# Kernel tuning notes

Hardware: AMD Instinct MI355X
Metric: run time of the kernel (lower is better)

Reference implementation:

```python
import jax, jax.numpy as jnp
import numpy as np

B1, B2, R, L, D, H = 48, 48, 36, 30, 1024, 4
EPS = 1e-8


def _l2norm(x):
    return x / (jnp.sqrt(jnp.sum(x * x, axis=-1, keepdims=True)) + EPS)


def _summary_attn(x, w1, b1, w2, b2):
    # x: (B1,B2,N,D). MLP scores -> softmax over N -> weighted mean over H heads.
    h = jax.nn.relu(jnp.einsum('abnd,ed->abne', x, w1) + b1)
    s = jnp.einsum('abne,he->abnh', h, w2) + b2          # (B1,B2,N,H)
    p = jax.nn.softmax(jnp.swapaxes(s, -1, -2), axis=-1)  # (B1,B2,H,N)
    w = jnp.einsum('abhn,abnd->abhd', p, x)               # (B1,B2,H,D)
    return w.mean(axis=-2)                                # (B1,B2,D)


def setup_inputs() -> dict:
    key = jax.random.key(0)
    ks = jax.random.split(key, 12)
    r = np.sqrt(6.0) / np.sqrt(D + D)  # xavier uniform as in init_weights
    return {
        'v1': jax.random.normal(ks[0], (B1, R, D), dtype=jnp.float32),
        'v2': jax.random.normal(ks[1], (B2, L, D), dtype=jnp.float32),
        'w_img': jax.random.uniform(ks[2], (D, D), jnp.float32, -r, r),
        'w_txt': jax.random.uniform(ks[3], (D, D), jnp.float32, -r, r),
        'w1a': jax.random.normal(ks[4], (D, D), jnp.float32) * 0.02,
        'b1a': jnp.zeros((D,), jnp.float32),
        'w2a': jax.random.normal(ks[5], (H, D), jnp.float32) * 0.02,
        'b2a': jnp.zeros((H,), jnp.float32),
        'w1b': jax.random.normal(ks[6], (D, D), jnp.float32) * 0.02,
        'b1b': jnp.zeros((D,), jnp.float32),
        'w2b': jax.random.normal(ks[7], (H, D), jnp.float32) * 0.02,
        'b2b': jnp.zeros((H,), jnp.float32),
    }


def reference(v1, v2, w_img, w_txt, w1a, b1a, w2a, b2a, w1b, b1b, w2b, b2b):
    d = v1.shape[-1]
    inv_sqrt_d = np.float32(1.0 / np.sqrt(d))
    k1 = jnp.einsum('ard,ed->are', v1, w_img)  # (B1,R,D)
    k2 = jnp.einsum('bld,ed->ble', v2, w_txt)  # (B2,L,D)

    # qkv_attention(k2, k1, v1): queries=words, keys/values=regions
    s1 = jnp.einsum('bld,ard->ablr', k2, k1) * inv_sqrt_d   # (B1,B2,L,R)
    p1 = jax.nn.softmax(s1, axis=-1)
    fused_v2 = jnp.einsum('ablr,ard->abld', p1, v1)         # weighted_v1 -> fused_v2

    # qkv_attention(k1, k2, v2): queries=regions, keys/values=words
    s2 = jnp.einsum('ard,bld->abrl', k1, k2) * inv_sqrt_d   # (B1,B2,R,L)
    p2 = jax.nn.softmax(s2, axis=-1)
    fused_v1 = jnp.einsum('abrl,bld->abrd', p2, v2)         # weighted_v2 -> fused_v1

    co_v1 = _l2norm(_summary_attn(fused_v1, w1a, b1a, w2a, b2a))
    co_v2 = _l2norm(_summary_attn(fused_v2, w1b, b1b, w2b, b2b))
    return jnp.sum(co_v1 * co_v2, axis=-1)  # (B1,B2) score matrix
```

## Files before the change

kernel.cpp:

```cpp
#include <hip/hip_runtime.h>

#define D 1024
#define NB1 48
#define NB2 48
#define RR 36
#define LL 30
#define NH 4

typedef short bf16x8 __attribute__((ext_vector_type(8)));
typedef float f32x4 __attribute__((ext_vector_type(4)));
typedef unsigned short u16x8 __attribute__((ext_vector_type(8)));

#define MFMA16(a, b, c) __builtin_amdgcn_mfma_f32_16x16x32_bf16(a, b, c, 0, 0, 0)

__device__ __forceinline__ unsigned short f2bf(float x) {
  unsigned u = __float_as_uint(x);
  u += 0x7FFF + ((u >> 16) & 1);
  return (unsigned short)(u >> 16);
}
__device__ __forceinline__ float bf2f(unsigned short h) {
  return __uint_as_float(((unsigned)h) << 16);
}
__device__ __forceinline__ void split8(const float* v, bf16x8& h8, bf16x8& l8) {
  u16x8 hi, lo;
#pragma unroll
  for (int i = 0; i < 8; ++i) {
    unsigned short h = f2bf(v[i]);
    hi[i] = h;
    lo[i] = f2bf(v[i] - bf2f(h));
  }
  h8 = __builtin_bit_cast(bf16x8, hi);
  l8 = __builtin_bit_cast(bf16x8, lo);
}

__device__ __forceinline__ void conv_body(const float* __restrict__ X,
                                          unsigned short* __restrict__ out,
                                          int rows, int g) {
  const int lane = threadIdx.x & 63;
  const int tile = g >> 5, kc = g & 31;
  const int row = tile * 16 + (lane & 15);
  const int k = kc * 32 + (lane >> 4) * 8;
  float v[8];
  if (row < rows) {
    const float4* s = (const float4*)(X + (size_t)row * 1024 + k);
    float4 x0 = s[0], x1 = s[1];
    v[0] = x0.x; v[1] = x0.y; v[2] = x0.z; v[3] = x0.w;
    v[4] = x1.x; v[5] = x1.y; v[6] = x1.z; v[7] = x1.w;
  } else {
#pragma unroll
    for (int i = 0; i < 8; ++i) v[i] = 0.f;
  }
  bf16x8 hi, lo;
  split8(v, hi, lo);
  bf16x8* o = (bf16x8*)(out + (size_t)g * 1024 + lane * 8);
  o[0] = hi;
  o[64] = lo;
}

__global__ __launch_bounds__(256) void conv6(
    const float* __restrict__ v1, const float* __restrict__ v2,
    const float* __restrict__ wimg, const float* __restrict__ wtxt,
    const float* __restrict__ w1a, const float* __restrict__ w1b,
    unsigned short* v1f, unsigned short* v2f, unsigned short* wimgf,
    unsigned short* wtxtf, unsigned short* w1af, unsigned short* w1bf) {
  const float* X; unsigned short* O; int rows;
  switch (blockIdx.y) {
    case 0: X = v1; O = v1f; rows = 1728; break;
    case 1: X = v2; O = v2f; rows = 1440; break;
    case 2: X = wimg; O = wimgf; rows = 1024; break;
    case 3: X = wtxt; O = wtxtf; rows = 1024; break;
    case 4: X = w1a; O = w1af; rows = 1024; break;
    default: X = w1b; O = w1bf; rows = 1024; break;
  }
  const int tiles = (rows + 15) >> 4;
  const int g = blockIdx.x * 4 + (threadIdx.x >> 6);
  if (g >= tiles * 32) return;
  conv_body(X, O, rows, g);
}

__global__ __launch_bounds__(256) void conv_k(const float* __restrict__ k1,
                                              const float* __restrict__ k2,
                                              unsigned short* k1f, unsigned short* k2f) {
  const float* X = blockIdx.y ? k2 : k1;
  unsigned short* O = blockIdx.y ? k2f : k1f;
  const int rows = blockIdx.y ? 1440 : 1728;
  const int tiles = (rows + 15) >> 4;
  const int g = blockIdx.x * 4 + (threadIdx.x >> 6);
  if (g >= tiles * 32) return;
  conv_body(X, O, rows, g);
}

__global__ __launch_bounds__(256) void convG(const float* __restrict__ G2a,
                                             const float* __restrict__ G1b,
                                             unsigned short* G2aF, unsigned short* G1bF) {
  const int t = threadIdx.x, lane = t & 63;
  const int bb = blockIdx.x >> 4;
  const int nt = ((blockIdx.x & 15) << 2) + (t >> 6);
  const int c = lane & 15, q = lane >> 4;
  if (blockIdx.y == 0) {
    float v[8];
#pragma unroll
    for (int j = 0; j < 8; ++j) {
      int l = q * 8 + j;
      v[j] = (l < LL) ? G2a[(size_t)(bb * LL + l) * D + nt * 16 + c] : 0.f;
    }
    bf16x8 hi, lo;
    split8(v, hi, lo);
    bf16x8* o = (bf16x8*)(G2aF + ((size_t)(bb * 64 + nt) * 2) * 512 + lane * 8);
    o[0] = hi;
    o[64] = lo;
  } else {
#pragma unroll
    for (int kc = 0; kc < 2; ++kc) {
      float v[8];
#pragma unroll
      for (int j = 0; j < 8; ++j) {
        int r = kc * 32 + q * 8 + j;
        v[j] = (r < RR) ? G1b[(size_t)(bb * RR + r) * D + nt * 16 + c] : 0.f;
      }
      bf16x8 hi, lo;
      split8(v, hi, lo);
      bf16x8* o = (bf16x8*)(G1bF + (((size_t)(bb * 64 + nt) * 2 + kc) * 2) * 512 + lane * 8);
      o[0] = hi;
      o[64] = lo;
    }
  }
}

__device__ __forceinline__ void gemm4_body(const bf16x8* __restrict__ Af,
                                           const bf16x8* __restrict__ Bf,
                                           float* __restrict__ C,
                                           int M, int N, float scale,
                                           int Mtiles, int Ntiles) {
  const int lane = threadIdx.x & 63;
  const int w = threadIdx.x >> 6;
  const int mb = blockIdx.y * 8 + (w >> 1) * 4;
  const int nb = blockIdx.x * 8 + (w & 1) * 4;
  size_t ab[4], bb[4];
#pragma unroll
  for (int i = 0; i < 4; ++i) {
    int tm = mb + i; if (tm > Mtiles - 1) tm = Mtiles - 1;
    ab[i] = (size_t)tm * 4096 + lane;
    int tn = nb + i; if (tn > Ntiles - 1) tn = Ntiles - 1;
    bb[i] = (size_t)tn * 4096 + lane;
  }
  f32x4 acc[4][4];
#pragma unroll
  for (int i = 0; i < 4; ++i)
#pragma unroll
    for (int j = 0; j < 4; ++j) acc[i][j] = (f32x4){0.f, 0.f, 0.f, 0.f};
#pragma unroll 1
  for (int kc = 0; kc < 32; ++kc) {
    bf16x8 ah[4], al[4], bh[4], bl[4];
#pragma unroll
    for (int i = 0; i < 4; ++i) { ah[i] = Af[ab[i]]; al[i] = Af[ab[i] + 64]; ab[i] += 128; }
#pragma unroll
    for (int j = 0; j < 4; ++j) { bh[j] = Bf[bb[j]]; bl[j] = Bf[bb[j] + 64]; bb[j] += 128; }
#pragma unroll
    for (int i = 0; i < 4; ++i)
#pragma unroll
      for (int j = 0; j < 4; ++j) {
        acc[i][j] = MFMA16(ah[i], bh[j], acc[i][j]);
        acc[i][j] = MFMA16(al[i], bh[j], acc[i][j]);
        acc[i][j] = MFMA16(ah[i], bl[j], acc[i][j]);
      }
  }
  const int c16 = lane & 15, q = lane >> 4;
#pragma unroll
  for (int i = 0; i < 4; ++i) {
#pragma unroll
    for (int reg = 0; reg < 4; ++reg) {
      int r = (mb + i) * 16 + q * 4 + reg;
      if (r < M) {
#pragma unroll
        for (int j = 0; j < 4; ++j) {
          int col = (nb + j) * 16 + c16;
          if (col < N) C[(size_t)r * N + col] = acc[i][j][reg] * scale;
        }
      }
    }
  }
}

__global__ __launch_bounds__(256) void proj_fused(
    const bf16x8* __restrict__ v1f, const bf16x8* __restrict__ v2f,
    const bf16x8* __restrict__ wimgf, const bf16x8* __restrict__ wtxtf,
    const bf16x8* __restrict__ w1af, const bf16x8* __restrict__ w1bf,
    float* k1, float* k2, float* G2a, float* G1b) {
  const int z = blockIdx.z;
  const bf16x8* Af = (z == 0 || z == 3) ? v1f : v2f;
  const bf16x8* Bf = (z == 0) ? wimgf : (z == 1) ? wtxtf : (z == 2) ? w1af : w1bf;
  float* C = (z == 0) ? k1 : (z == 1) ? k2 : (z == 2) ? G2a : G1b;
  const int M = (z == 0 || z == 3) ? 1728 : 1440;
  const int Mt = (z == 0 || z == 3) ? 108 : 92;
  if ((int)blockIdx.y * 8 >= Mt) return;
  gemm4_body(Af, Bf, C, M, 1024, 1.f, Mt, 64);
}

__global__ __launch_bounds__(256) void cross_fused(
    const bf16x8* __restrict__ k2f, const bf16x8* __restrict__ k1f,
    const bf16x8* __restrict__ v2f, const bf16x8* __restrict__ v1f,
    float* Sbuf, float* Cbuf) {
  if (blockIdx.z == 0) gemm4_body(k2f, k1f, Sbuf, 1440, 1728, 0.03125f, 92, 108);
  else                 gemm4_body(v2f, v1f, Cbuf, 1440, 1728, 1.f, 92, 108);
}

__global__ __launch_bounds__(256) void gram_partial(const float* __restrict__ v1,
                                                    const float* __restrict__ v2,
                                                    float* __restrict__ pg) {
  const int y = blockIdx.y, cx = blockIdx.x;
  const int isV1 = y < 48;
  const int batch = isV1 ? y : y - 48;
  const int Nr = isV1 ? RR : LL;
  const float* base = isV1 ? v1 + (size_t)batch * RR * D : v2 + (size_t)batch * LL * D;
  __shared__ __align__(16) float vs[36][132];
  const int t = threadIdx.x;
  for (int idx = t; idx < Nr * 32; idx += 256) {
    int row = idx >> 5, c4 = idx & 31;
    *(float4*)&vs[row][c4 * 4] = *(const float4*)&base[(size_t)row * D + cx * 128 + c4 * 4];
  }
  __syncthreads();
  const int nt3 = Nr / 3;
  float acc[3][3] = {{0.f,0.f,0.f},{0.f,0.f,0.f},{0.f,0.f,0.f}};
  const int i0 = (t / nt3) * 3, j0 = (t - (t / nt3) * nt3) * 3;
  if (t < nt3 * nt3) {
    for (int k4 = 0; k4 < 32; ++k4) {
      float4 a[3], b[3];
#pragma unroll
      for (int ii = 0; ii < 3; ++ii) a[ii] = *(const float4*)&vs[i0 + ii][k4 * 4];
#pragma unroll
      for (int jj = 0; jj < 3; ++jj) b[jj] = *(const float4*)&vs[j0 + jj][k4 * 4];
#pragma unroll
      for (int ii = 0; ii < 3; ++ii)
#pragma unroll
        for (int jj = 0; jj < 3; ++jj) {
          acc[ii][jj] = fmaf(a[ii].x, b[jj].x, acc[ii][jj]);
          acc[ii][jj] = fmaf(a[ii].y, b[jj].y, acc[ii][jj]);
          acc[ii][jj] = fmaf(a[ii].z, b[jj].z, acc[ii][jj]);
          acc[ii][jj] = fmaf(a[ii].w, b[jj].w, acc[ii][jj]);
        }
    }
    float* o = pg + ((size_t)y * 8 + cx) * 1296;
#pragma unroll
    for (int ii = 0; ii < 3; ++ii)
#pragma unroll
      for (int jj = 0; jj < 3; ++jj) o[(i0 + ii) * Nr + (j0 + jj)] = acc[ii][jj];
  }
}

__global__ __launch_bounds__(256) void gram_reduce(const float* __restrict__ pg,
                                                   float* __restrict__ g11,
                                                   float* __restrict__ g22) {
  const int y = blockIdx.x;
  const int isV1 = y < 48;
  const int batch = isV1 ? y : y - 48;
  const int NN = isV1 ? RR * RR : LL * LL;
  const float* p = pg + (size_t)y * 8 * 1296;
  float* o = isV1 ? g11 + (size_t)batch * RR * RR : g22 + (size_t)batch * LL * LL;
  for (int i = threadIdx.x; i < NN; i += 256) {
    float s = 0.f;
#pragma unroll
    for (int c = 0; c < 8; ++c) s += p[c * 1296 + i];
    o[i] = s;
  }
}

__global__ __launch_bounds__(256) void pair_kernel(
    const float* __restrict__ Sb, const float* __restrict__ Cb,
    const bf16x8* __restrict__ G2aF, const bf16x8* __restrict__ G1bF,
    const float* __restrict__ g22, const float* __restrict__ g11,
    const float* __restrict__ b1a, const float* __restrict__ w2a, const float* __restrict__ b2a,
    const float* __restrict__ b1b, const float* __restrict__ w2b, const float* __restrict__ b2b,
    float* __restrict__ out) {
  const int pair = blockIdx.x;
  const int a = pair / NB2;
  const int b = pair - a * NB2;
  const int t = threadIdx.x, lane = t & 63, w = t >> 6;
  const int c16 = lane & 15, q = lane >> 4;

  __shared__ __align__(16) float sS[LL][RR];
  __shared__ __align__(16) float p2s[48][36];
  __shared__ __align__(16) float p1s[32][68];
  __shared__ float red[4][48][NH];
  __shared__ float sa[RR][NH];
  __shared__ float sbm[LL][NH];
  __shared__ float qa[RR], qb[LL], u1[RR], u2[LL];
  __shared__ float redbuf[3][4];

  for (int i = t; i < 48 * 36; i += 256) ((float*)p2s)[i] = 0.f;
  for (int i = t; i < 32 * 68; i += 256) ((float*)p1s)[i] = 0.f;
  for (int i = t; i < LL * RR; i += 256) {
    int l = i / RR, r = i - l * RR;
    sS[l][r] = Sb[(size_t)(b * LL + l) * 1728 + a * RR + r];
  }
  __syncthreads();

  if (t < LL) {
    float m = -1e30f;
    for (int r = 0; r < RR; ++r) m = fmaxf(m, sS[t][r]);
    float s = 0.f;
    for (int r = 0; r < RR; ++r) { float e = __expf(sS[t][r] - m); p1s[t][r] = e; s += e; }
    float inv = 1.f / s;
    for (int r = 0; r < RR; ++r) p1s[t][r] *= inv;
  } else if (t >= 64 && t < 64 + RR) {
    int r = t - 64;
    float m = -1e30f;
    for (int l = 0; l < LL; ++l) m = fmaxf(m, sS[l][r]);
    float s = 0.f;
    for (int l = 0; l < LL; ++l) { float e = __expf(sS[l][r] - m); p2s[r][l] = e; s += e; }
    float inv = 1.f / s;
    for (int l = 0; l < LL; ++l) p2s[r][l] *= inv;
  }
  __syncthreads();

  bf16x8 pAh[3], pAl[3];
#pragma unroll
  for (int mt = 0; mt < 3; ++mt) {
    float v[8];
    const float* rp = &p2s[mt * 16 + c16][q * 8];
    float4 x0 = *(const float4*)rp;
    float4 x1 = *(const float4*)(rp + 4);
    v[0] = x0.x; v[1] = x0.y; v[2] = x0.z; v[3] = x0.w;
    v[4] = x1.x; v[5] = x1.y; v[6] = x1.z; v[7] = x1.w;
    split8(v, pAh[mt], pAl[mt]);
  }
  float scA[3][4][NH];
#pragma unroll
  for (int mt = 0; mt < 3; ++mt)
#pragma unroll
    for (int reg = 0; reg < 4; ++reg)
#pragma unroll
      for (int h = 0; h < NH; ++h) scA[mt][reg][h] = 0.f;

  for (int nt = w; nt < 64; nt += 4) {
    const bf16x8* gp = G2aF + ((size_t)(b * 64 + nt) * 2) * 64 + lane;
    bf16x8 Bh = gp[0], Bl = gp[64];
    const int col = nt * 16 + c16;
    const float bias = b1a[col];
    const float w0 = w2a[col], w1 = w2a[D + col], w2v = w2a[2 * D + col], w3 = w2a[3 * D + col];
#pragma unroll
    for (int mt = 0; mt < 3; ++mt) {
      f32x4 acc = {bias, bias, bias, bias};
      acc = MFMA16(pAh[mt], Bh, acc);
      acc = MFMA16(pAl[mt], Bh, acc);
      acc = MFMA16(pAh[mt], Bl, acc);
#pragma unroll
      for (int reg = 0; reg < 4; ++reg) {
        float hv = fmaxf(acc[reg], 0.f);
        scA[mt][reg][0] = fmaf(hv, w0, scA[mt][reg][0]);
        scA[mt][reg][1] = fmaf(hv, w1, scA[mt][reg][1]);
        scA[mt][reg][2] = fmaf(hv, w2v, scA[mt][reg][2]);
        scA[mt][reg][3] = fmaf(hv, w3, scA[mt][reg][3]);
      }
    }
  }
#pragma unroll
  for (int mt = 0; mt < 3; ++mt)
#pragma unroll
    for (int reg = 0; reg < 4; ++reg)
#pragma unroll
      for (int h = 0; h < NH; ++h) {
        float v = scA[mt][reg][h];
        v += __shfl_xor(v, 1);
        v += __shfl_xor(v, 2);
        v += __shfl_xor(v, 4);
        v += __shfl_xor(v, 8);
        if (c16 == 0) red[w][mt * 16 + q * 4 + reg][h] = v;
      }
  __syncthreads();
  if (t < RR * NH) {
    int r = t >> 2, h = t & 3;
    sa[r][h] = red[0][r][h] + red[1][r][h] + red[2][r][h] + red[3][r][h] + b2a[h];
  }
  __syncthreads();

  bf16x8 pBh[2][2], pBl[2][2];
#pragma unroll
  for (int mt = 0; mt < 2; ++mt)
#pragma unroll
    for (int kc = 0; kc < 2; ++kc) {
      float v[8];
      const float* rp = &p1s[mt * 16 + c16][kc * 32 + q * 8];
      float4 x0 = *(const float4*)rp;
      float4 x1 = *(const float4*)(rp + 4);
      v[0] = x0.x; v[1] = x0.y; v[2] = x0.z; v[3] = x0.w;
      v[4] = x1.x; v[5] = x1.y; v[6] = x1.z; v[7] = x1.w;
      split8(v, pBh[mt][kc], pBl[mt][kc]);
    }
  float scB[2][4][NH];
#pragma unroll
  for (int mt = 0; mt < 2; ++mt)
#pragma unroll
    for (int reg = 0; reg < 4; ++reg)
#pragma unroll
      for (int h = 0; h < NH; ++h) scB[mt][reg][h] = 0.f;

  for (int nt = w; nt < 64; nt += 4) {
    const bf16x8* gp = G1bF + (((size_t)(a * 64 + nt) * 2) * 2) * 64 + lane;
    bf16x8 B0h = gp[0], B0l = gp[64], B1h = gp[128], B1l = gp[192];
    const int col = nt * 16 + c16;
    const float bias = b1b[col];
    const float w0 = w2b[col], w1 = w2b[D + col], w2v = w2b[2 * D + col], w3 = w2b[3 * D + col];
#pragma unroll
    for (int mt = 0; mt < 2; ++mt) {
      f32x4 acc = {bias, bias, bias, bias};
      acc = MFMA16(pBh[mt][0], B0h, acc);
      acc = MFMA16(pBl[mt][0], B0h, acc);
      acc = MFMA16(pBh[mt][0], B0l, acc);
      acc = MFMA16(pBh[mt][1], B1h, acc);
      acc = MFMA16(pBl[mt][1], B1h, acc);
      acc = MFMA16(pBh[mt][1], B1l, acc);
#pragma unroll
      for (int reg = 0; reg < 4; ++reg) {
        float hv = fmaxf(acc[reg], 0.f);
        scB[mt][reg][0] = fmaf(hv, w0, scB[mt][reg][0]);
        scB[mt][reg][1] = fmaf(hv, w1, scB[mt][reg][1]);
        scB[mt][reg][2] = fmaf(hv, w2v, scB[mt][reg][2]);
        scB[mt][reg][3] = fmaf(hv, w3, scB[mt][reg][3]);
      }
    }
  }
#pragma unroll
  for (int mt = 0; mt < 2; ++mt)
#pragma unroll
    for (int reg = 0; reg < 4; ++reg)
#pragma unroll
      for (int h = 0; h < NH; ++h) {
        float v = scB[mt][reg][h];
        v += __shfl_xor(v, 1);
        v += __shfl_xor(v, 2);
        v += __shfl_xor(v, 4);
        v += __shfl_xor(v, 8);
        if (c16 == 0) red[w][mt * 16 + q * 4 + reg][h] = v;
      }
  __syncthreads();
  if (t < LL * NH) {
    int l = t >> 2, h = t & 3;
    sbm[l][h] = red[0][l][h] + red[1][l][h] + red[2][l][h] + red[3][l][h] + b2b[h];
  }
  __syncthreads();

  if (t < NH) {
    const int h = t;
    float m = -1e30f;
    for (int r = 0; r < RR; ++r) m = fmaxf(m, sa[r][h]);
    float s = 0.f;
    for (int r = 0; r < RR; ++r) { float e = __expf(sa[r][h] - m); sa[r][h] = e; s += e; }
    float inv = 1.f / s;
    for (int r = 0; r < RR; ++r) sa[r][h] *= inv;
  } else if (t >= 64 && t < 64 + NH) {
    const int h = t - 64;
    float m = -1e30f;
    for (int l = 0; l < LL; ++l) m = fmaxf(m, sbm[l][h]);
    float s = 0.f;
    for (int l = 0; l < LL; ++l) { float e = __expf(sbm[l][h] - m); sbm[l][h] = e; s += e; }
    float inv = 1.f / s;
    for (int l = 0; l < LL; ++l) sbm[l][h] *= inv;
  }
  __syncthreads();
  if (t < RR) qa[t] = 0.25f * (sa[t][0] + sa[t][1] + sa[t][2] + sa[t][3]);
  else if (t >= 64 && t < 64 + LL) {
    int l = t - 64;
    qb[l] = 0.25f * (sbm[l][0] + sbm[l][1] + sbm[l][2] + sbm[l][3]);
  }
  __syncthreads();

  if (t < LL) {
    float x = 0.f;
    for (int r = 0; r < RR; ++r) x = fmaf(qa[r], p2s[r][t], x);
    u2[t] = x;
  } else if (t >= 64 && t < 64 + RR) {
    int r = t - 64;
    float x = 0.f;
    for (int l = 0; l < LL; ++l) x = fmaf(qb[l], p1s[l][r], x);
    u1[r] = x;
  }
  __syncthreads();

  float pnum = 0.f, pn1 = 0.f, pn2 = 0.f;
  {
    const float* Cab = Cb + (size_t)(b * LL) * 1728 + a * RR;
    for (int i = t; i < LL * RR; i += 256) {
      int l = i / RR, r = i - l * RR;
      pnum = fmaf(u2[l] * u1[r], Cab[(size_t)l * 1728 + r], pnum);
    }
    const float* G22 = g22 + (size_t)b * LL * LL;
    for (int i = t; i < LL * LL; i += 256) {
      int l = i / LL, l2 = i - l * LL;
      pn1 = fmaf(u2[l] * u2[l2], G22[i], pn1);
    }
    const float* G11 = g11 + (size_t)a * RR * RR;
    for (int i = t; i < RR * RR; i += 256) {
      int r = i / RR, r2 = i - r * RR;
      pn2 = fmaf(u1[r] * u1[r2], G11[i], pn2);
    }
  }
#pragma unroll
  for (int off = 32; off > 0; off >>= 1) {
    pnum += __shfl_down(pnum, off);
    pn1  += __shfl_down(pn1, off);
    pn2  += __shfl_down(pn2, off);
  }
  if ((t & 63) == 0) { redbuf[0][w] = pnum; redbuf[1][w] = pn1; redbuf[2][w] = pn2; }
  __syncthreads();
  if (t == 0) {
    float num = redbuf[0][0] + redbuf[0][1] + redbuf[0][2] + redbuf[0][3];
    float n1s = redbuf[1][0] + redbuf[1][1] + redbuf[1][2] + redbuf[1][3];
    float n2s = redbuf[2][0] + redbuf[2][1] + redbuf[2][2] + redbuf[2][3];
    float n1 = sqrtf(fmaxf(n1s, 0.f));
    float n2 = sqrtf(fmaxf(n2s, 0.f));
    out[pair] = num / ((n1 + 1e-8f) * (n2 + 1e-8f));
  }
}

extern "C" void kernel_launch(void* const* d_in, const int* in_sizes, int n_in,
                              void* d_out, int out_size, void* d_ws, size_t ws_size,
                              hipStream_t stream) {
  const float* v1    = (const float*)d_in[0];
  const float* v2    = (const float*)d_in[1];
  const float* w_img = (const float*)d_in[2];
  const float* w_txt = (const float*)d_in[3];
  const float* w1a   = (const float*)d_in[4];
  const float* b1a   = (const float*)d_in[5];
  const float* w2a   = (const float*)d_in[6];
  const float* b2a   = (const float*)d_in[7];
  const float* w1b   = (const float*)d_in[8];
  const float* b1b   = (const float*)d_in[9];
  const float* w2b   = (const float*)d_in[10];
  const float* b2b   = (const float*)d_in[11];
  float* out = (float*)d_out;

  float* ws   = (float*)d_ws;
  float* k1   = ws;
  float* k2   = k1 + (size_t)1728 * 1024;
  float* G2a  = k2 + (size_t)1440 * 1024;
  float* G1b  = G2a + (size_t)1440 * 1024;
  float* Sbuf = G1b + (size_t)1728 * 1024;
  float* Cbuf = Sbuf + (size_t)1440 * 1728;
  float* g22  = Cbuf + (size_t)1440 * 1728;
  float* g11  = g22 + (size_t)48 * 900;

  unsigned short* fb    = (unsigned short*)(g11 + (size_t)48 * 1296);
  unsigned short* v1f   = fb;
  unsigned short* v2f   = v1f + (size_t)108 * 32768;
  unsigned short* k1f   = v2f + (size_t)92 * 32768;
  unsigned short* k2f   = k1f + (size_t)108 * 32768;
  unsigned short* wimgf = k2f + (size_t)92 * 32768;
  unsigned short* wtxtf = wimgf + (size_t)64 * 32768;
  unsigned short* w1af  = wtxtf + (size_t)64 * 32768;
  unsigned short* w1bf  = w1af + (size_t)64 * 32768;
  unsigned short* G2aF  = w1bf + (size_t)64 * 32768;
  unsigned short* G1bF  = G2aF + (size_t)48 * 65536;

  float* pg = (float*)k1f;

  conv6<<<dim3(864, 6), 256, 0, stream>>>(v1, v2, w_img, w_txt, w1a, w1b,
                                          v1f, v2f, wimgf, wtxtf, w1af, w1bf);
  gram_partial<<<dim3(8, 96), 256, 0, stream>>>(v1, v2, pg);
  gram_reduce<<<96, 256, 0, stream>>>(pg, g11, g22);

  proj_fused<<<dim3(8, 14, 4), 256, 0, stream>>>(
      (const bf16x8*)v1f, (const bf16x8*)v2f, (const bf16x8*)wimgf,
      (const bf16x8*)wtxtf, (const bf16x8*)w1af, (const bf16x8*)w1bf,
      k1, k2, G2a, G1b);

  conv_k<<<dim3(864, 2), 256, 0, stream>>>(k1, k2, k1f, k2f);
  convG<<<dim3(768, 2), 256, 0, stream>>>(G2a, G1b, G2aF, G1bF);

  cross_fused<<<dim3(14, 12, 2), 256, 0, stream>>>(
      (const bf16x8*)k2f, (const bf16x8*)k1f, (const bf16x8*)v2f, (const bf16x8*)v1f,
      Sbuf, Cbuf);

  pair_kernel<<<2304, 256, 0, stream>>>(Sbuf, Cbuf, (const bf16x8*)G2aF, (const bf16x8*)G1bF,
                                        g22, g11, b1a, w2a, b2a, b1b, w2b, b2b, out);
}
```

Measured before the change: 339.7 us.

## Batch summary-MLP scoring across pairs sharing G fragments; merge post-projection conversions

```diff
diff --git a/kernel.cpp b/kernel.cpp
--- a/kernel.cpp
+++ b/kernel.cpp
@@ -10,22 +10,23 @@
 typedef short bf16x8 __attribute__((ext_vector_type(8)));
 typedef float f32x4 __attribute__((ext_vector_type(4)));
 typedef unsigned short u16x8 __attribute__((ext_vector_type(8)));
+typedef unsigned short ush;
 
 #define MFMA16(a, b, c) __builtin_amdgcn_mfma_f32_16x16x32_bf16(a, b, c, 0, 0, 0)
 
-__device__ __forceinline__ unsigned short f2bf(float x) {
+__device__ __forceinline__ ush f2bf(float x) {
   unsigned u = __float_as_uint(x);
   u += 0x7FFF + ((u >> 16) & 1);
-  return (unsigned short)(u >> 16);
-}
-__device__ __forceinline__ float bf2f(unsigned short h) {
+  return (ush)(u >> 16);
+}
+__device__ __forceinline__ float bf2f(ush h) {
   return __uint_as_float(((unsigned)h) << 16);
 }
 __device__ __forceinline__ void split8(const float* v, bf16x8& h8, bf16x8& l8) {
   u16x8 hi, lo;
 #pragma unroll
   for (int i = 0; i < 8; ++i) {
-    unsigned short h = f2bf(v[i]);
+    ush h = f2bf(v[i]);
     hi[i] = h;
     lo[i] = f2bf(v[i] - bf2f(h));
   }
@@ -34,7 +35,7 @@
 }
 
 __device__ __forceinline__ void conv_body(const float* __restrict__ X,
-                                          unsigned short* __restrict__ out,
+                                          ush* __restrict__ out,
                                           int rows, int g) {
   const int lane = threadIdx.x & 63;
   const int tile = g >> 5, kc = g & 31;
@@ -61,9 +62,8 @@
     const float* __restrict__ v1, const float* __restrict__ v2,
     const float* __restrict__ wimg, const float* __restrict__ wtxt,
     const float* __restrict__ w1a, const float* __restrict__ w1b,
-    unsigned short* v1f, unsigned short* v2f, unsigned short* wimgf,
-    unsigned short* wtxtf, unsigned short* w1af, unsigned short* w1bf) {
-  const float* X; unsigned short* O; int rows;
+    ush* v1f, ush* v2f, ush* wimgf, ush* wtxtf, ush* w1af, ush* w1bf) {
+  const float* X; ush* O; int rows;
   switch (blockIdx.y) {
     case 0: X = v1; O = v1f; rows = 1728; break;
     case 1: X = v2; O = v2f; rows = 1440; break;
@@ -78,26 +78,25 @@
   conv_body(X, O, rows, g);
 }
 
-__global__ __launch_bounds__(256) void conv_k(const float* __restrict__ k1,
-                                              const float* __restrict__ k2,
-                                              unsigned short* k1f, unsigned short* k2f) {
-  const float* X = blockIdx.y ? k2 : k1;
-  unsigned short* O = blockIdx.y ? k2f : k1f;
-  const int rows = blockIdx.y ? 1440 : 1728;
-  const int tiles = (rows + 15) >> 4;
-  const int g = blockIdx.x * 4 + (threadIdx.x >> 6);
-  if (g >= tiles * 32) return;
-  conv_body(X, O, rows, g);
-}
-
-__global__ __launch_bounds__(256) void convG(const float* __restrict__ G2a,
-                                             const float* __restrict__ G1b,
-                                             unsigned short* G2aF, unsigned short* G1bF) {
+__global__ __launch_bounds__(256) void conv_post(
+    const float* __restrict__ k1, const float* __restrict__ k2,
+    const float* __restrict__ G2a, const float* __restrict__ G1b,
+    ush* k1f, ush* k2f, ush* G2aF, ush* G1bF) {
+  const int bid = blockIdx.x;
   const int t = threadIdx.x, lane = t & 63;
-  const int bb = blockIdx.x >> 4;
-  const int nt = ((blockIdx.x & 15) << 2) + (t >> 6);
-  const int c = lane & 15, q = lane >> 4;
-  if (blockIdx.y == 0) {
+  if (bid < 1728) {
+    const float* X = (bid >= 864) ? k2 : k1;
+    ush* O = (bid >= 864) ? k2f : k1f;
+    const int rows = (bid >= 864) ? 1440 : 1728;
+    const int bx = (bid >= 864) ? bid - 864 : bid;
+    const int tiles = (rows + 15) >> 4;
+    const int g = bx * 4 + (t >> 6);
+    if (g < tiles * 32) conv_body(X, O, rows, g);
+  } else if (bid < 2496) {
+    const int x = bid - 1728;
+    const int bb = x >> 4;
+    const int nt = ((x & 15) << 2) + (t >> 6);
+    const int c = lane & 15, q = lane >> 4;
     float v[8];
 #pragma unroll
     for (int j = 0; j < 8; ++j) {
@@ -110,17 +109,21 @@
     o[0] = hi;
     o[64] = lo;
   } else {
+    const int x = bid - 2496;
+    const int aa = x >> 4;
+    const int nt = ((x & 15) << 2) + (t >> 6);
+    const int c = lane & 15, q = lane >> 4;
 #pragma unroll
     for (int kc = 0; kc < 2; ++kc) {
       float v[8];
 #pragma unroll
       for (int j = 0; j < 8; ++j) {
         int r = kc * 32 + q * 8 + j;
-        v[j] = (r < RR) ? G1b[(size_t)(bb * RR + r) * D + nt * 16 + c] : 0.f;
+        v[j] = (r < RR) ? G1b[(size_t)(aa * RR + r) * D + nt * 16 + c] : 0.f;
       }
       bf16x8 hi, lo;
       split8(v, hi, lo);
-      bf16x8* o = (bf16x8*)(G1bF + (((size_t)(bb * 64 + nt) * 2 + kc) * 2) * 512 + lane * 8);
+      bf16x8* o = (bf16x8*)(G1bF + (((size_t)(aa * 64 + nt) * 2 + kc) * 2) * 512 + lane * 8);
       o[0] = hi;
       o[64] = lo;
     }
@@ -265,34 +268,220 @@
   }
 }
 
-__global__ __launch_bounds__(256) void pair_kernel(
+__global__ __launch_bounds__(256) void score_kernel(
+    const float* __restrict__ Sb,
+    const bf16x8* __restrict__ G2aF, const bf16x8* __restrict__ G1bF,
+    const float* __restrict__ b1a, const float* __restrict__ w2a,
+    const float* __restrict__ b1b, const float* __restrict__ w2b,
+    float* __restrict__ saBuf, float* __restrict__ sbBuf) {
+  __shared__ ush frag[24576];
+  const int t = threadIdx.x, lane = t & 63, w = t >> 6;
+  const int c16 = lane & 15, q = lane >> 4;
+  const int bid = blockIdx.x;
+
+  for (int i = t; i < 3072; i += 256) ((int4*)frag)[i] = make_int4(0, 0, 0, 0);
+  __syncthreads();
+
+  if (bid < 288) {
+    const int b = bid / 6, ag = bid % 6;
+    for (int cc = t; cc < 8 * RR; cc += 256) {
+      const int pp = cc / RR, r = cc - pp * RR;
+      const int a = ag * 8 + pp;
+      const float* sp = Sb + (size_t)(b * LL) * 1728 + a * RR + r;
+      float v[LL];
+      float m = -1e30f;
+#pragma unroll
+      for (int l = 0; l < LL; ++l) { v[l] = sp[(size_t)l * 1728]; m = fmaxf(m, v[l]); }
+      float s = 0.f;
+#pragma unroll
+      for (int l = 0; l < LL; ++l) { v[l] = __expf(v[l] - m); s += v[l]; }
+      const float inv = 1.f / s;
+      ush* base = frag + (pp * 3 + (r >> 4)) * 1024;
+      const int mr = r & 15;
+#pragma unroll
+      for (int l = 0; l < LL; ++l) {
+        float p = v[l] * inv;
+        ush hi = f2bf(p);
+        ush lo = f2bf(p - bf2f(hi));
+        int idx = (((l >> 3) * 16 + mr) << 3) + (l & 7);
+        base[idx] = hi; base[512 + idx] = lo;
+      }
+    }
+    __syncthreads();
+    const int nt0 = w * 16;
+#pragma unroll 1
+    for (int g = 0; g < 4; ++g) {
+      bf16x8 Ah[6], Al[6];
+#pragma unroll
+      for (int i = 0; i < 6; ++i) {
+        const ush* p = frag + (g * 6 + i) * 1024 + lane * 8;
+        Ah[i] = *(const bf16x8*)p;
+        Al[i] = *(const bf16x8*)(p + 512);
+      }
+      float scP[6][4][4];
+#pragma unroll
+      for (int i = 0; i < 6; ++i)
+#pragma unroll
+        for (int reg = 0; reg < 4; ++reg)
+#pragma unroll
+          for (int h = 0; h < NH; ++h) scP[i][reg][h] = 0.f;
+#pragma unroll 2
+      for (int nt = nt0; nt < nt0 + 16; ++nt) {
+        const bf16x8* gp = G2aF + (size_t)(b * 64 + nt) * 128 + lane;
+        bf16x8 Bh = gp[0], Bl = gp[64];
+        const int col = nt * 16 + c16;
+        const float bias = b1a[col];
+        const float w0 = w2a[col], w1 = w2a[D + col], w2v = w2a[2 * D + col], w3 = w2a[3 * D + col];
+#pragma unroll
+        for (int i = 0; i < 6; ++i) {
+          f32x4 acc = {bias, bias, bias, bias};
+          acc = MFMA16(Ah[i], Bh, acc);
+          acc = MFMA16(Al[i], Bh, acc);
+          acc = MFMA16(Ah[i], Bl, acc);
+#pragma unroll
+          for (int reg = 0; reg < 4; ++reg) {
+            float hv = fmaxf(acc[reg], 0.f);
+            scP[i][reg][0] = fmaf(hv, w0, scP[i][reg][0]);
+            scP[i][reg][1] = fmaf(hv, w1, scP[i][reg][1]);
+            scP[i][reg][2] = fmaf(hv, w2v, scP[i][reg][2]);
+            scP[i][reg][3] = fmaf(hv, w3, scP[i][reg][3]);
+          }
+        }
+      }
+#pragma unroll
+      for (int i = 0; i < 6; ++i) {
+        const int T = g * 6 + i, pp = T / 3, mtl = T - pp * 3;
+        const int pair = (ag * 8 + pp) * 48 + b;
+#pragma unroll
+        for (int reg = 0; reg < 4; ++reg) {
+          const int r = mtl * 16 + q * 4 + reg;
+#pragma unroll
+          for (int h = 0; h < NH; ++h) {
+            float v = scP[i][reg][h];
+            v += __shfl_xor(v, 1); v += __shfl_xor(v, 2);
+            v += __shfl_xor(v, 4); v += __shfl_xor(v, 8);
+            if (c16 == 0 && r < RR) atomicAdd(&saBuf[(size_t)pair * 144 + r * 4 + h], v);
+          }
+        }
+      }
+    }
+  } else {
+    const int bid2 = bid - 288;
+    const int a = bid2 / 8, bg = bid2 % 8;
+    for (int cc = t; cc < 6 * LL; cc += 256) {
+      const int pp = cc / LL, l = cc - pp * LL;
+      const int b = bg * 6 + pp;
+      const float* sp = Sb + (size_t)(b * LL + l) * 1728 + a * RR;
+      float v[RR];
+      float m = -1e30f;
+#pragma unroll
+      for (int r = 0; r < RR; ++r) { v[r] = sp[r]; m = fmaxf(m, v[r]); }
+      float s = 0.f;
+#pragma unroll
+      for (int r = 0; r < RR; ++r) { v[r] = __expf(v[r] - m); s += v[r]; }
+      const float inv = 1.f / s;
+      ush* base = frag + ((pp * 2 + (l >> 4)) * 2) * 1024;
+      const int mr = l & 15;
+#pragma unroll
+      for (int r = 0; r < RR; ++r) {
+        float p = v[r] * inv;
+        ush hi = f2bf(p);
+        ush lo = f2bf(p - bf2f(hi));
+        const int kc = r >> 5, k = r & 31;
+        int idx = kc * 1024 + (((k >> 3) * 16 + mr) << 3) + (k & 7);
+        base[idx] = hi; base[512 + idx] = lo;
+      }
+    }
+    __syncthreads();
+    const int nt0 = w * 16;
+#pragma unroll 1
+    for (int g = 0; g < 4; ++g) {
+      bf16x8 A0h[3], A0l[3], A1h[3], A1l[3];
+#pragma unroll
+      for (int i = 0; i < 3; ++i) {
+        const ush* p = frag + (g * 3 + i) * 2048 + lane * 8;
+        A0h[i] = *(const bf16x8*)p;
+        A0l[i] = *(const bf16x8*)(p + 512);
+        A1h[i] = *(const bf16x8*)(p + 1024);
+        A1l[i] = *(const bf16x8*)(p + 1536);
+      }
+      float scP[3][4][4];
+#pragma unroll
+      for (int i = 0; i < 3; ++i)
+#pragma unroll
+        for (int reg = 0; reg < 4; ++reg)
+#pragma unroll
+          for (int h = 0; h < NH; ++h) scP[i][reg][h] = 0.f;
+#pragma unroll 2
+      for (int nt = nt0; nt < nt0 + 16; ++nt) {
+        const bf16x8* gp = G1bF + (size_t)(a * 64 + nt) * 256 + lane;
+        bf16x8 B0h = gp[0], B0l = gp[64], B1h = gp[128], B1l = gp[192];
+        const int col = nt * 16 + c16;
+        const float bias = b1b[col];
+        const float w0 = w2b[col], w1 = w2b[D + col], w2v = w2b[2 * D + col], w3 = w2b[3 * D + col];
+#pragma unroll
+        for (int i = 0; i < 3; ++i) {
+          f32x4 acc = {bias, bias, bias, bias};
+          acc = MFMA16(A0h[i], B0h, acc);
+          acc = MFMA16(A0l[i], B0h, acc);
+          acc = MFMA16(A0h[i], B0l, acc);
+          acc = MFMA16(A1h[i], B1h, acc);
+          acc = MFMA16(A1l[i], B1h, acc);
+          acc = MFMA16(A1h[i], B1l, acc);
+#pragma unroll
+          for (int reg = 0; reg < 4; ++reg) {
+            float hv = fmaxf(acc[reg], 0.f);
+            scP[i][reg][0] = fmaf(hv, w0, scP[i][reg][0]);
+            scP[i][reg][1] = fmaf(hv, w1, scP[i][reg][1]);
+            scP[i][reg][2] = fmaf(hv, w2v, scP[i][reg][2]);
+            scP[i][reg][3] = fmaf(hv, w3, scP[i][reg][3]);
+          }
+        }
+      }
+#pragma unroll
+      for (int i = 0; i < 3; ++i) {
+        const int T = g * 3 + i, pp = T >> 1, mtl = T & 1;
+        const int pair = a * 48 + bg * 6 + pp;
+#pragma unroll
+        for (int reg = 0; reg < 4; ++reg) {
+          const int l = mtl * 16 + q * 4 + reg;
+#pragma unroll
+          for (int h = 0; h < NH; ++h) {
+            float v = scP[i][reg][h];
+            v += __shfl_xor(v, 1); v += __shfl_xor(v, 2);
+            v += __shfl_xor(v, 4); v += __shfl_xor(v, 8);
+            if (c16 == 0 && l < LL) atomicAdd(&sbBuf[(size_t)pair * 120 + l * 4 + h], v);
+          }
+        }
+      }
+    }
+  }
+}
+
+__global__ __launch_bounds__(256) void finalize_kernel(
     const float* __restrict__ Sb, const float* __restrict__ Cb,
-    const bf16x8* __restrict__ G2aF, const bf16x8* __restrict__ G1bF,
     const float* __restrict__ g22, const float* __restrict__ g11,
-    const float* __restrict__ b1a, const float* __restrict__ w2a, const float* __restrict__ b2a,
-    const float* __restrict__ b1b, const float* __restrict__ w2b, const float* __restrict__ b2b,
+    const float* __restrict__ saBuf, const float* __restrict__ sbBuf,
     float* __restrict__ out) {
   const int pair = blockIdx.x;
   const int a = pair / NB2;
   const int b = pair - a * NB2;
-  const int t = threadIdx.x, lane = t & 63, w = t >> 6;
-  const int c16 = lane & 15, q = lane >> 4;
-
-  __shared__ __align__(16) float sS[LL][RR];
-  __shared__ __align__(16) float p2s[48][36];
-  __shared__ __align__(16) float p1s[32][68];
-  __shared__ float red[4][48][NH];
+  const int t = threadIdx.x, w = t >> 6;
+
+  __shared__ float sS[LL][RR];
+  __shared__ float p1s[LL][RR];
+  __shared__ float p2s[RR][32];
   __shared__ float sa[RR][NH];
   __shared__ float sbm[LL][NH];
   __shared__ float qa[RR], qb[LL], u1[RR], u2[LL];
   __shared__ float redbuf[3][4];
 
-  for (int i = t; i < 48 * 36; i += 256) ((float*)p2s)[i] = 0.f;
-  for (int i = t; i < 32 * 68; i += 256) ((float*)p1s)[i] = 0.f;
   for (int i = t; i < LL * RR; i += 256) {
     int l = i / RR, r = i - l * RR;
     sS[l][r] = Sb[(size_t)(b * LL + l) * 1728 + a * RR + r];
   }
+  if (t < RR * NH) ((float*)sa)[t] = saBuf[(size_t)pair * 144 + t];
+  if (t >= 128 && t < 128 + LL * NH) ((float*)sbm)[t - 128] = sbBuf[(size_t)pair * 120 + (t - 128)];
   __syncthreads();
 
   if (t < LL) {
@@ -310,146 +499,16 @@
     for (int l = 0; l < LL; ++l) { float e = __expf(sS[l][r] - m); p2s[r][l] = e; s += e; }
     float inv = 1.f / s;
     for (int l = 0; l < LL; ++l) p2s[r][l] *= inv;
-  }
-  __syncthreads();
-
-  bf16x8 pAh[3], pAl[3];
-#pragma unroll
-  for (int mt = 0; mt < 3; ++mt) {
-    float v[8];
-    const float* rp = &p2s[mt * 16 + c16][q * 8];
-    float4 x0 = *(const float4*)rp;
-    float4 x1 = *(const float4*)(rp + 4);
-    v[0] = x0.x; v[1] = x0.y; v[2] = x0.z; v[3] = x0.w;
-    v[4] = x1.x; v[5] = x1.y; v[6] = x1.z; v[7] = x1.w;
-    split8(v, pAh[mt], pAl[mt]);
-  }
-  float scA[3][4][NH];
-#pragma unroll
-  for (int mt = 0; mt < 3; ++mt)
-#pragma unroll
-    for (int reg = 0; reg < 4; ++reg)
-#pragma unroll
-      for (int h = 0; h < NH; ++h) scA[mt][reg][h] = 0.f;
-
-  for (int nt = w; nt < 64; nt += 4) {
-    const bf16x8* gp = G2aF + ((size_t)(b * 64 + nt) * 2) * 64 + lane;
-    bf16x8 Bh = gp[0], Bl = gp[64];
-    const int col = nt * 16 + c16;
-    const float bias = b1a[col];
-    const float w0 = w2a[col], w1 = w2a[D + col], w2v = w2a[2 * D + col], w3 = w2a[3 * D + col];
-#pragma unroll
-    for (int mt = 0; mt < 3; ++mt) {
-      f32x4 acc = {bias, bias, bias, bias};
-      acc = MFMA16(pAh[mt], Bh, acc);
-      acc = MFMA16(pAl[mt], Bh, acc);
-      acc = MFMA16(pAh[mt], Bl, acc);
-#pragma unroll
-      for (int reg = 0; reg < 4; ++reg) {
-        float hv = fmaxf(acc[reg], 0.f);
-        scA[mt][reg][0] = fmaf(hv, w0, scA[mt][reg][0]);
-        scA[mt][reg][1] = fmaf(hv, w1, scA[mt][reg][1]);
-        scA[mt][reg][2] = fmaf(hv, w2v, scA[mt][reg][2]);
-        scA[mt][reg][3] = fmaf(hv, w3, scA[mt][reg][3]);
-      }
-    }
-  }
-#pragma unroll
-  for (int mt = 0; mt < 3; ++mt)
-#pragma unroll
-    for (int reg = 0; reg < 4; ++reg)
-#pragma unroll
-      for (int h = 0; h < NH; ++h) {
-        float v = scA[mt][reg][h];
-        v += __shfl_xor(v, 1);
-        v += __shfl_xor(v, 2);
-        v += __shfl_xor(v, 4);
-        v += __shfl_xor(v, 8);
-        if (c16 == 0) red[w][mt * 16 + q * 4 + reg][h] = v;
-      }
-  __syncthreads();
-  if (t < RR * NH) {
-    int r = t >> 2, h = t & 3;
-    sa[r][h] = red[0][r][h] + red[1][r][h] + red[2][r][h] + red[3][r][h] + b2a[h];
-  }
-  __syncthreads();
-
-  bf16x8 pBh[2][2], pBl[2][2];
-#pragma unroll
-  for (int mt = 0; mt < 2; ++mt)
-#pragma unroll
-    for (int kc = 0; kc < 2; ++kc) {
-      float v[8];
-      const float* rp = &p1s[mt * 16 + c16][kc * 32 + q * 8];
-      float4 x0 = *(const float4*)rp;
-      float4 x1 = *(const float4*)(rp + 4);
-      v[0] = x0.x; v[1] = x0.y; v[2] = x0.z; v[3] = x0.w;
-      v[4] = x1.x; v[5] = x1.y; v[6] = x1.z; v[7] = x1.w;
-      split8(v, pBh[mt][kc], pBl[mt][kc]);
-    }
-  float scB[2][4][NH];
-#pragma unroll
-  for (int mt = 0; mt < 2; ++mt)
-#pragma unroll
-    for (int reg = 0; reg < 4; ++reg)
-#pragma unroll
-      for (int h = 0; h < NH; ++h) scB[mt][reg][h] = 0.f;
-
-  for (int nt = w; nt < 64; nt += 4) {
-    const bf16x8* gp = G1bF + (((size_t)(a * 64 + nt) * 2) * 2) * 64 + lane;
-    bf16x8 B0h = gp[0], B0l = gp[64], B1h = gp[128], B1l = gp[192];
-    const int col = nt * 16 + c16;
-    const float bias = b1b[col];
-    const float w0 = w2b[col], w1 = w2b[D + col], w2v = w2b[2 * D + col], w3 = w2b[3 * D + col];
-#pragma unroll
-    for (int mt = 0; mt < 2; ++mt) {
-      f32x4 acc = {bias, bias, bias, bias};
-      acc = MFMA16(pBh[mt][0], B0h, acc);
-      acc = MFMA16(pBl[mt][0], B0h, acc);
-      acc = MFMA16(pBh[mt][0], B0l, acc);
-      acc = MFMA16(pBh[mt][1], B1h, acc);
-      acc = MFMA16(pBl[mt][1], B1h, acc);
-      acc = MFMA16(pBh[mt][1], B1l, acc);
-#pragma unroll
-      for (int reg = 0; reg < 4; ++reg) {
-        float hv = fmaxf(acc[reg], 0.f);
-        scB[mt][reg][0] = fmaf(hv, w0, scB[mt][reg][0]);
-        scB[mt][reg][1] = fmaf(hv, w1, scB[mt][reg][1]);
-        scB[mt][reg][2] = fmaf(hv, w2v, scB[mt][reg][2]);
-        scB[mt][reg][3] = fmaf(hv, w3, scB[mt][reg][3]);
-      }
-    }
-  }
-#pragma unroll
-  for (int mt = 0; mt < 2; ++mt)
-#pragma unroll
-    for (int reg = 0; reg < 4; ++reg)
-#pragma unroll
-      for (int h = 0; h < NH; ++h) {
-        float v = scB[mt][reg][h];
-        v += __shfl_xor(v, 1);
-        v += __shfl_xor(v, 2);
-        v += __shfl_xor(v, 4);
-        v += __shfl_xor(v, 8);
-        if (c16 == 0) red[w][mt * 16 + q * 4 + reg][h] = v;
-      }
-  __syncthreads();
-  if (t < LL * NH) {
-    int l = t >> 2, h = t & 3;
-    sbm[l][h] = red[0][l][h] + red[1][l][h] + red[2][l][h] + red[3][l][h] + b2b[h];
-  }
-  __syncthreads();
-
-  if (t < NH) {
-    const int h = t;
+  } else if (t >= 128 && t < 128 + NH) {
+    const int h = t - 128;
     float m = -1e30f;
     for (int r = 0; r < RR; ++r) m = fmaxf(m, sa[r][h]);
     float s = 0.f;
     for (int r = 0; r < RR; ++r) { float e = __expf(sa[r][h] - m); sa[r][h] = e; s += e; }
     float inv = 1.f / s;
     for (int r = 0; r < RR; ++r) sa[r][h] *= inv;
-  } else if (t >= 64 && t < 64 + NH) {
-    const int h = t - 64;
+  } else if (t >= 192 && t < 192 + NH) {
+    const int h = t - 192;
     float m = -1e30f;
     for (int l = 0; l < LL; ++l) m = fmaxf(m, sbm[l][h]);
     float s = 0.f;
@@ -523,11 +582,9 @@
   const float* w1a   = (const float*)d_in[4];
   const float* b1a   = (const float*)d_in[5];
   const float* w2a   = (const float*)d_in[6];
-  const float* b2a   = (const float*)d_in[7];
   const float* w1b   = (const float*)d_in[8];
   const float* b1b   = (const float*)d_in[9];
   const float* w2b   = (const float*)d_in[10];
-  const float* b2b   = (const float*)d_in[11];
   float* out = (float*)d_out;
 
   float* ws   = (float*)d_ws;
@@ -540,19 +597,23 @@
   float* g22  = Cbuf + (size_t)1440 * 1728;
   float* g11  = g22 + (size_t)48 * 900;
 
-  unsigned short* fb    = (unsigned short*)(g11 + (size_t)48 * 1296);
-  unsigned short* v1f   = fb;
-  unsigned short* v2f   = v1f + (size_t)108 * 32768;
-  unsigned short* k1f   = v2f + (size_t)92 * 32768;
-  unsigned short* k2f   = k1f + (size_t)108 * 32768;
-  unsigned short* wimgf = k2f + (size_t)92 * 32768;
-  unsigned short* wtxtf = wimgf + (size_t)64 * 32768;
-  unsigned short* w1af  = wtxtf + (size_t)64 * 32768;
-  unsigned short* w1bf  = w1af + (size_t)64 * 32768;
-  unsigned short* G2aF  = w1bf + (size_t)64 * 32768;
-  unsigned short* G1bF  = G2aF + (size_t)48 * 65536;
+  ush* fb    = (ush*)(g11 + (size_t)48 * 1296);
+  ush* v1f   = fb;
+  ush* v2f   = v1f + (size_t)108 * 32768;
+  ush* k1f   = v2f + (size_t)92 * 32768;
+  ush* k2f   = k1f + (size_t)108 * 32768;
+  ush* wimgf = k2f + (size_t)92 * 32768;
+  ush* wtxtf = wimgf + (size_t)64 * 32768;
+  ush* w1af  = wtxtf + (size_t)64 * 32768;
+  ush* w1bf  = w1af + (size_t)64 * 32768;
+  ush* G2aF  = w1bf + (size_t)64 * 32768;
+  ush* G1bF  = G2aF + (size_t)48 * 65536;
+  float* saBuf = (float*)(G1bF + (size_t)48 * 131072);
+  float* sbBuf = saBuf + (size_t)2304 * 144;
 
   float* pg = (float*)k1f;
+
+  hipMemsetAsync(saBuf, 0, (size_t)2304 * (144 + 120) * sizeof(float), stream);
 
   conv6<<<dim3(864, 6), 256, 0, stream>>>(v1, v2, w_img, w_txt, w1a, w1b,
                                           v1f, v2f, wimgf, wtxtf, w1af, w1bf);
@@ -564,13 +625,14 @@
       (const bf16x8*)wtxtf, (const bf16x8*)w1af, (const bf16x8*)w1bf,
       k1, k2, G2a, G1b);
 
-  conv_k<<<dim3(864, 2), 256, 0, stream>>>(k1, k2, k1f, k2f);
-  convG<<<dim3(768, 2), 256, 0, stream>>>(G2a, G1b, G2aF, G1bF);
+  conv_post<<<3264, 256, 0, stream>>>(k1, k2, G2a, G1b, k1f, k2f, G2aF, G1bF);
 
   cross_fused<<<dim3(14, 12, 2), 256, 0, stream>>>(
       (const bf16x8*)k2f, (const bf16x8*)k1f, (const bf16x8*)v2f, (const bf16x8*)v1f,
       Sbuf, Cbuf);
 
-  pair_kernel<<<2304, 256, 0, stream>>>(Sbuf, Cbuf, (const bf16x8*)G2aF, (const bf16x8*)G1bF,
-                                        g22, g11, b1a, w2a, b2a, b1b, w2b, b2b, out);
-}
+  score_kernel<<<672, 256, 0, stream>>>(Sbuf, (const bf16x8*)G2aF, (const bf16x8*)G1bF,
+                                        b1a, w2a, b1b, w2b, saBuf, sbBuf);
+
+  finalize_kernel<<<2304, 256, 0, stream>>>(Sbuf, Cbuf, g22, g11, saBuf, sbBuf, out);
+}
```

Measured after the change: 499.6 us. 1.47x slower.
